# Kernel optimization log

Measured on AMD Instinct MI355X. Metric: run time of the kernel, lower is better.

Reference implementation:

```python
import jax, jax.numpy as jnp
import numpy as np

B, S, H, N_ITEMS = 1024, 200, 256, 50000


def setup_inputs() -> dict:
    key = jax.random.key(0)
    ks = jax.random.split(key, 10)
    s = 0.05
    x = jax.random.randint(ks[0], (B, S), 0, N_ITEMS)
    # timestamps: increasing along the sequence
    t = jnp.sort(jax.random.uniform(ks[1], (B, S), dtype=jnp.float32) * 10.0, axis=1)
    item_emb = (jax.random.normal(ks[2], (N_ITEMS, H), dtype=jnp.float32) * s).at[0].set(0.0)  # padding_idx=0
    W_ih = jax.random.normal(ks[3], (3 * H, H), dtype=jnp.float32) * s
    W_hh = jax.random.normal(ks[4], (3 * H, H), dtype=jnp.float32) * s
    b_ih = jnp.zeros((3 * H,), jnp.float32)
    b_hh = jnp.zeros((3 * H,), jnp.float32)
    W1 = jax.random.normal(ks[5], (H, H), dtype=jnp.float32) * s
    b1 = jnp.zeros((H,), jnp.float32)
    W2 = jax.random.normal(ks[6], (H, H), dtype=jnp.float32) * s
    b2 = jnp.zeros((H,), jnp.float32)
    W_head = jax.random.normal(ks[7], (N_ITEMS, H), dtype=jnp.float32) * s
    b_head = jnp.zeros((N_ITEMS,), jnp.float32)
    return dict(x=x, t=t, item_emb=item_emb, W_ih=W_ih, W_hh=W_hh, b_ih=b_ih,
                b_hh=b_hh, W1=W1, b1=b1, W2=W2, b2=b2, W_head=W_head, b_head=b_head)


def _gru_cell(xe, h, W_ih, W_hh, b_ih, b_hh):
    # PyTorch GRUCell: gates ordered (r, z, n)
    gi = xe @ W_ih.T + b_ih  # [B, 3H]
    gh = h @ W_hh.T + b_hh
    i_r, i_z, i_n = jnp.split(gi, 3, axis=-1)
    h_r, h_z, h_n = jnp.split(gh, 3, axis=-1)
    r = jax.nn.sigmoid(i_r + h_r)
    z = jax.nn.sigmoid(i_z + h_z)
    n = jnp.tanh(i_n + r * h_n)
    return (1.0 - z) * n + z * h


def _ode_f(h, W1, b1, W2, b2):
    # ODEFunc: MLP on hidden state (t-independent)
    return jnp.tanh(h @ W1.T + b1) @ W2.T + b2


def _rk4_step(h, dt, W1, b1, W2, b2):
    # dt: [B, 1]; dt == 0 on the last step => identity (matches i < seq_len-1 guard)
    f = lambda hh: _ode_f(hh, W1, b1, W2, b2)
    k1 = f(h)
    k2 = f(h + 0.5 * dt * k1)
    k3 = f(h + 0.5 * dt * k2)
    k4 = f(h + dt * k3)
    return h + (dt / 6.0) * (k1 + 2.0 * k2 + 2.0 * k3 + k4)


def reference(x, t, item_emb, W_ih, W_hh, b_ih, b_hh, W1, b1, W2, b2, W_head, b_head):
    x_emb = item_emb[x]  # [B, S, H]
    bsz = x.shape[0]
    # dt_i = max(t_{i+1}, t_i + 1e-5) - t_i for i < S-1, 0 for the final step
    t_next = jnp.maximum(t[:, 1:], t[:, :-1] + 1e-5)
    dt = jnp.concatenate([t_next - t[:, :-1], jnp.zeros((bsz, 1), t.dtype)], axis=1)  # [B, S]
    xs = (jnp.swapaxes(x_emb, 0, 1), jnp.swapaxes(dt, 0, 1)[..., None])  # [S,B,H], [S,B,1]
    h0 = jnp.zeros((bsz, x_emb.shape[-1]), x_emb.dtype)

    def step(h, inp):
        xe, dts = inp
        h = _gru_cell(xe, h, W_ih, W_hh, b_ih, b_hh)
        h = _rk4_step(h, dts, W1, b1, W2, b2)
        return h, None

    h, _ = jax.lax.scan(step, h0, xs)
    return h @ W_head.T + b_head  # [B, n_items]
```

## Files before the change

kernel.cpp:

```cpp
#include <hip/hip_runtime.h>


#define B_SZ   1024
#define S_LEN  200
#define HD     256
#define NITEMS 50000
#define NPAD   50048

#define OFF_WHH 0
#define OFF_WIH 196608
#define OFF_W1  393216
#define OFF_W2  458752
#define OFF_BHH 524288
#define OFF_BIH 525056
#define OFF_B1  525824
#define OFF_B2  526080
#define CANON_N 526336

typedef short short8 __attribute__((ext_vector_type(8)));
typedef float f32x4  __attribute__((ext_vector_type(4)));

__device__ __forceinline__ float bf2f(unsigned short u){
  unsigned v = ((unsigned)u) << 16; float f; __builtin_memcpy(&f, &v, 4); return f;
}
__device__ __forceinline__ unsigned short f2bf(float f){
  unsigned u; __builtin_memcpy(&u, &f, 4);
  u += 0x7FFFu + ((u >> 16) & 1u);
  return (unsigned short)(u >> 16);
}
__device__ __forceinline__ float fsig(float x){ return 1.0f / (1.0f + __expf(-x)); }
__device__ __forceinline__ float ftanh(float x){
  float e = __expf(-2.0f * fabsf(x));
  float r = (1.0f - e) / (1.0f + e);
  return copysignf(r, x);
}
__device__ __forceinline__ f32x4 MFMA(short8 a, short8 b, f32x4 c){
  return __builtin_amdgcn_mfma_f32_16x16x32_bf16(a, b, c, 0, 0, 0);
}
__device__ __forceinline__ int foff(int kc, int row){
  return (kc * 16 + ((row ^ kc) & 15)) * 8;
}

__global__ void sniff_kernel(const unsigned short* __restrict__ t, int* __restrict__ flag){
  int lane = threadIdx.x & 63;
  int bad = 0;
#pragma unroll
  for (int q = 0; q < 8; ++q)
    if (t[lane * 8 + q] > 0x4200u) bad = 1;
  unsigned long long m = __ballot(bad);
  if (lane == 0) flag[0] = (m != 0ull) ? 1 : 0;
}

__global__ void conv_kernel(const int* __restrict__ flag,
    const void* __restrict__ Whh, const void* __restrict__ Wih,
    const void* __restrict__ W1,  const void* __restrict__ W2,
    const void* __restrict__ bhh, const void* __restrict__ bih,
    const void* __restrict__ b1,  const void* __restrict__ b2,
    unsigned short* __restrict__ dst)
{
  int i = blockIdx.x * 256 + threadIdx.x;
  if (i >= CANON_N) return;
  int f32m = flag[0];
  const void* src; int off = i;
  if (i < OFF_WIH)      { src = Whh; off = i - OFF_WHH; }
  else if (i < OFF_W1)  { src = Wih; off = i - OFF_WIH; }
  else if (i < OFF_W2)  { src = W1;  off = i - OFF_W1; }
  else if (i < OFF_BHH) { src = W2;  off = i - OFF_W2; }
  else if (i < OFF_BIH) { src = bhh; off = i - OFF_BHH; }
  else if (i < OFF_B1)  { src = bih; off = i - OFF_BIH; }
  else if (i < OFF_B2)  { src = b1;  off = i - OFF_B1; }
  else                  { src = b2;  off = i - OFF_B2; }
  unsigned short v = f32m ? f2bf(((const float*)src)[off])
                          : ((const unsigned short*)src)[off];
  dst[i] = v;
}

__global__ void convw_kernel(const int* __restrict__ flag,
    const void* __restrict__ Wh, unsigned short* __restrict__ dst)
{
  int i4 = blockIdx.x * 256 + threadIdx.x;
  if (i4 * 4 >= NITEMS * HD) return;
  if (flag[0]){
    f32x4 v = ((const f32x4*)Wh)[i4];
#pragma unroll
    for (int q = 0; q < 4; ++q) dst[i4 * 4 + q] = f2bf(v[q]);
  } else {
    ((unsigned long long*)dst)[i4] = ((const unsigned long long*)Wh)[i4];
  }
}

__global__ void dt_kernel(const void* __restrict__ t, const int* __restrict__ flag,
                          float* __restrict__ dt){
  int i = blockIdx.x * 256 + threadIdx.x;
  if (i >= B_SZ * S_LEN) return;
  int f32m = flag[0];
  int s = i % S_LEN;
  float tc = f32m ? ((const float*)t)[i] : bf2f(((const unsigned short*)t)[i]);
  float d = 0.0f;
  if (s < S_LEN - 1){
    float tn = f32m ? ((const float*)t)[i + 1] : bf2f(((const unsigned short*)t)[i + 1]);
    d = fmaxf(tn, tc + 1e-5f) - tc;
  }
  dt[i] = d;
}

__global__ __launch_bounds__(256) void gitems_kernel(
    const void* __restrict__ emb, const unsigned short* __restrict__ canon,
    const int* __restrict__ flag, void* __restrict__ tbl, int tblf32)
{
  __shared__ __align__(16) short ap[4][4096];
  const int tid = threadIdx.x;
  const int i0 = blockIdx.x * 64;
  const int n0 = blockIdx.y * 256;
  const int f32m = flag[0];
  {
    int kc = tid & 31, r8 = tid >> 5;
#pragma unroll
    for (int p = 0; p < 8; ++p){
      int row = p * 8 + r8;
      int gr = i0 + row; if (gr > NITEMS - 1) gr = NITEMS - 1;
      short8 v;
      if (f32m){
        const f32x4* src = (const f32x4*)((const float*)emb + gr * HD + kc * 8);
        f32x4 v0 = src[0], v1 = src[1];
#pragma unroll
        for (int q = 0; q < 4; ++q){ v[q] = (short)f2bf(v0[q]); v[4+q] = (short)f2bf(v1[q]); }
      } else {
        v = *(const short8*)((const unsigned short*)emb + gr * HD + kc * 8);
      }
      *(short8*)&ap[row >> 4][foff(kc, row & 15)] = v;
    }
  }
  __syncthreads();
  const int wave = tid >> 6, lane = tid & 63, col = lane & 15, quad = lane >> 4;
  const unsigned short* Wih = canon + OFF_WIH;
  const unsigned short* bih = canon + OFF_BIH;
  f32x4 zz = {0.0f, 0.0f, 0.0f, 0.0f};
  f32x4 acc[4][4];
#pragma unroll
  for (int rt = 0; rt < 4; ++rt)
#pragma unroll
    for (int ct = 0; ct < 4; ++ct) acc[rt][ct] = zz;

#pragma unroll
  for (int ks = 0; ks < 8; ++ks){
    short8 bf[4];
#pragma unroll
    for (int ct = 0; ct < 4; ++ct){
      int n = n0 + wave * 64 + ct * 16 + col;
      bf[ct] = *(const short8*)(Wih + n * HD + ks * 32 + quad * 8);
    }
    int kc = ks * 4 + quad;
#pragma unroll
    for (int rt = 0; rt < 4; ++rt){
      short8 a = *(const short8*)&ap[rt][foff(kc, col)];
#pragma unroll
      for (int ct = 0; ct < 4; ++ct) acc[rt][ct] = MFMA(a, bf[ct], acc[rt][ct]);
    }
  }
  float bv[4];
#pragma unroll
  for (int ct = 0; ct < 4; ++ct) bv[ct] = bf2f(bih[n0 + wave * 64 + ct * 16 + col]);
  float* tfo = (float*)tbl; unsigned short* tbo = (unsigned short*)tbl;
#pragma unroll
  for (int rt = 0; rt < 4; ++rt)
#pragma unroll
    for (int ct = 0; ct < 4; ++ct)
#pragma unroll
      for (int r = 0; r < 4; ++r){
        int row = i0 + rt * 16 + quad * 4 + r;
        if (row < NITEMS){
          int n = n0 + wave * 64 + ct * 16 + col;
          float v = acc[rt][ct][r] + bv[ct];
          if (tblf32) tfo[row * 768 + n] = v;
          else        tbo[row * 768 + n] = (unsigned short)f2bf(v);
        }
      }
}

__global__ __launch_bounds__(512)
void scan_kernel(
    const int* __restrict__ x, const float* __restrict__ dtp,
    const unsigned short* __restrict__ canon,
    const void* __restrict__ tbl, int tblf32,
    float* __restrict__ hstate)
{
  __shared__ __align__(16) short bufhi[2][4096];
  __shared__ __align__(16) short buflo[2][4096];
  __shared__ __align__(16) int   xl[16 * S_LEN];
  __shared__ __align__(16) float dtall[16 * S_LEN];

  const int tid  = threadIdx.x;
  const int wave = tid >> 6;
  const int lane = tid & 63;
  const int col  = lane & 15;
  const int quad = lane >> 4;
  const int r0   = blockIdx.x * 16;
  const int wc0  = wave * 32;

  const unsigned short* Whh = canon + OFF_WHH;
  const unsigned short* W1w = canon + OFF_W1;
  const unsigned short* W2w = canon + OFF_W2;
  const unsigned short* bhh = canon + OFF_BHH;
  const unsigned short* b1v = canon + OFF_B1;
  const unsigned short* b2v = canon + OFF_B2;

  {
    short8 z = {0,0,0,0,0,0,0,0};
    *(short8*)&bufhi[0][tid * 8] = z;
    *(short8*)&buflo[0][tid * 8] = z;
  }
  for (int i = tid; i < 16 * S_LEN; i += 512){
    xl[i]    = x[r0 * S_LEN + i];
    dtall[i] = dtp[r0 * S_LEN + i];
  }

  float bR[2], bZ[2], bN[2], b1c[2], b2c[2];
#pragma unroll
  for (int ct = 0; ct < 2; ++ct){
    int c = wc0 + ct * 16 + col;
    bR[ct]  = bf2f(bhh[c]);          bZ[ct] = bf2f(bhh[HD + c]);
    bN[ct]  = bf2f(bhh[2 * HD + c]);
    b1c[ct] = bf2f(b1v[c]);          b2c[ct] = bf2f(b2v[c]);
  }

  float h[2][4];
#pragma unroll
  for (int ct = 0; ct < 2; ++ct)
#pragma unroll
    for (int r = 0; r < 4; ++r) h[ct][r] = 0.0f;

  const float* tf = (const float*)tbl;
  const unsigned short* tb = (const unsigned short*)tbl;

  __syncthreads();

  for (int s = 0; s < S_LEN; ++s){
    const int pb = s & 1;
    float dtr[4];
#pragma unroll
    for (int r = 0; r < 4; ++r) dtr[r] = dtall[(quad * 4 + r) * S_LEN + s];

    f32x4 aR[2], aZ[2], aN[2];
    float giN[2][4];
#pragma unroll
    for (int r = 0; r < 4; ++r){
      int row = quad * 4 + r;
      long base = (long)xl[row * S_LEN + s] * 768;
#pragma unroll
      for (int ct = 0; ct < 2; ++ct){
        int c = wc0 + ct * 16 + col;
        float gr, gz, gn;
        if (tblf32){
          gr = __builtin_nontemporal_load(tf + base + c);
          gz = __builtin_nontemporal_load(tf + base + 256 + c);
          gn = __builtin_nontemporal_load(tf + base + 512 + c);
        } else {
          gr = bf2f(__builtin_nontemporal_load(tb + base + c));
          gz = bf2f(__builtin_nontemporal_load(tb + base + 256 + c));
          gn = bf2f(__builtin_nontemporal_load(tb + base + 512 + c));
        }
        aR[ct][r] = gr; aZ[ct][r] = gz; aN[ct][r] = 0.0f; giN[ct][r] = gn;
      }
    }
#pragma unroll
    for (int ks = 0; ks < 8; ++ks){
      int kc = ks * 4 + quad;
      short8 ahi = *(const short8*)&bufhi[pb][foff(kc, col)];
      short8 alo = *(const short8*)&buflo[pb][foff(kc, col)];
#pragma unroll
      for (int ct = 0; ct < 2; ++ct){
        int nb = wc0 + ct * 16 + col;
        short8 b0 = *(const short8*)(Whh + (0 * HD + nb) * HD + ks * 32 + quad * 8);
        aR[ct] = MFMA(ahi, b0, aR[ct]); aR[ct] = MFMA(alo, b0, aR[ct]);
        short8 b1f = *(const short8*)(Whh + (1 * HD + nb) * HD + ks * 32 + quad * 8);
        aZ[ct] = MFMA(ahi, b1f, aZ[ct]); aZ[ct] = MFMA(alo, b1f, aZ[ct]);
        short8 b2f = *(const short8*)(Whh + (2 * HD + nb) * HD + ks * 32 + quad * 8);
        aN[ct] = MFMA(ahi, b2f, aN[ct]); aN[ct] = MFMA(alo, b2f, aN[ct]);
      }
    }
    float hg[2][4], ksum[2][4];
#pragma unroll
    for (int ct = 0; ct < 2; ++ct)
#pragma unroll
      for (int r = 0; r < 4; ++r){
        int row = quad * 4 + r;
        float rr = fsig(aR[ct][r] + bR[ct]);
        float z_ = fsig(aZ[ct][r] + bZ[ct]);
        float nn = ftanh(giN[ct][r] + rr * (aN[ct][r] + bN[ct]));
        float hgv = (1.0f - z_) * nn + z_ * h[ct][r];
        hg[ct][r] = hgv;
        int c = wc0 + ct * 16 + col;
        bufhi[1 - pb][foff(c >> 3, row) + (c & 7)] = (short)f2bf(hgv);
      }
    __syncthreads();

#pragma unroll
    for (int j = 0; j < 4; ++j){
      f32x4 ua[2];
      ua[0] = (f32x4){b1c[0], b1c[0], b1c[0], b1c[0]};
      ua[1] = (f32x4){b1c[1], b1c[1], b1c[1], b1c[1]};
#pragma unroll
      for (int ks = 0; ks < 8; ++ks){
        int kc = ks * 4 + quad;
        short8 a = *(const short8*)&bufhi[1 - pb][foff(kc, col)];
#pragma unroll
        for (int ct = 0; ct < 2; ++ct){
          short8 w = *(const short8*)(W1w + (wc0 + ct * 16 + col) * HD + ks * 32 + quad * 8);
          ua[ct] = MFMA(a, w, ua[ct]);
        }
      }
#pragma unroll
      for (int ct = 0; ct < 2; ++ct)
#pragma unroll
        for (int r = 0; r < 4; ++r){
          int row = quad * 4 + r, c = wc0 + ct * 16 + col;
          bufhi[pb][foff(c >> 3, row) + (c & 7)] = (short)f2bf(ftanh(ua[ct][r]));
        }
      __syncthreads();

      f32x4 ka[2];
      ka[0] = (f32x4){b2c[0], b2c[0], b2c[0], b2c[0]};
      ka[1] = (f32x4){b2c[1], b2c[1], b2c[1], b2c[1]};
#pragma unroll
      for (int ks = 0; ks < 8; ++ks){
        int kc = ks * 4 + quad;
        short8 a = *(const short8*)&bufhi[pb][foff(kc, col)];
#pragma unroll
        for (int ct = 0; ct < 2; ++ct){
          short8 w = *(const short8*)(W2w + (wc0 + ct * 16 + col) * HD + ks * 32 + quad * 8);
          ka[ct] = MFMA(a, w, ka[ct]);
        }
      }
#pragma unroll
      for (int ct = 0; ct < 2; ++ct)
#pragma unroll
        for (int r = 0; r < 4; ++r){
          int row = quad * 4 + r;
          float dtv = dtr[r];
          float kv = ka[ct][r];
          int c = wc0 + ct * 16 + col;
          if (j == 0){
            ksum[ct][r] = kv;
            float y = hg[ct][r] + 0.5f * dtv * kv;
            bufhi[1 - pb][foff(c >> 3, row) + (c & 7)] = (short)f2bf(y);
          } else if (j == 1){
            ksum[ct][r] += 2.0f * kv;
            float y = hg[ct][r] + 0.5f * dtv * kv;
            bufhi[1 - pb][foff(c >> 3, row) + (c & 7)] = (short)f2bf(y);
          } else if (j == 2){
            ksum[ct][r] += 2.0f * kv;
            float y = hg[ct][r] + dtv * kv;
            bufhi[1 - pb][foff(c >> 3, row) + (c & 7)] = (short)f2bf(y);
          } else {
            ksum[ct][r] += kv;
            float hn = hg[ct][r] + (dtv * (1.0f / 6.0f)) * ksum[ct][r];
            h[ct][r] = hn;
            unsigned short hh = f2bf(hn);
            float fh = bf2f(hh);
            unsigned short hl = f2bf(hn - fh);
            bufhi[1 - pb][foff(c >> 3, row) + (c & 7)] = (short)hh;
            buflo[1 - pb][foff(c >> 3, row) + (c & 7)] = (short)hl;
          }
        }
      __syncthreads();
    }
  }
#pragma unroll
  for (int ct = 0; ct < 2; ++ct)
#pragma unroll
    for (int r = 0; r < 4; ++r){
      int row = quad * 4 + r;
      hstate[(r0 + row) * HD + wc0 + ct * 16 + col] = h[ct][r];
    }
}

__global__ __launch_bounds__(256) void head_kernel(
    const float* __restrict__ hstate,
    const unsigned short* __restrict__ Whb,
    const void* __restrict__ Wh,
    const void* __restrict__ bh, const int* __restrict__ flag, int wbf,
    void* __restrict__ outv)
{
  __shared__ __align__(16) short ahi[4][4096];
  __shared__ __align__(16) short alo[4][4096];
  const int tid = threadIdx.x;
  const int i0 = blockIdx.x * 64;
  const int n0 = blockIdx.y * 256;
  const int f32m = flag[0];
  {
    int kc = tid & 31, r8 = tid >> 5;
#pragma unroll
    for (int p = 0; p < 8; ++p){
      int row = p * 8 + r8;
      const float* src = hstate + (i0 + row) * HD + kc * 8;
      short8 vh, vl;
#pragma unroll
      for (int q = 0; q < 8; ++q){
        float f = src[q];
        unsigned short hb = f2bf(f);
        float fh = bf2f(hb);
        vh[q] = (short)hb; vl[q] = (short)f2bf(f - fh);
      }
      int off = foff(kc, row & 15);
      *(short8*)&ahi[row >> 4][off] = vh;
      *(short8*)&alo[row >> 4][off] = vl;
    }
  }
  __syncthreads();
  const int wave = tid >> 6, lane = tid & 63, col = lane & 15, quad = lane >> 4;
  f32x4 zz = {0.0f, 0.0f, 0.0f, 0.0f};
  f32x4 acc[4][4];
#pragma unroll
  for (int rt = 0; rt < 4; ++rt)
#pragma unroll
    for (int ct = 0; ct < 4; ++ct) acc[rt][ct] = zz;

  int nidx[4];
#pragma unroll
  for (int ct = 0; ct < 4; ++ct){
    int n = n0 + wave * 64 + ct * 16 + col;
    nidx[ct] = (n < NITEMS) ? n : (NITEMS - 1);
  }
#pragma unroll
  for (int ks = 0; ks < 8; ++ks){
    short8 bf[4];
#pragma unroll
    for (int ct = 0; ct < 4; ++ct){
      if (wbf){
        bf[ct] = *(const short8*)(Whb + nidx[ct] * HD + ks * 32 + quad * 8);
      } else if (f32m){
        const f32x4* src = (const f32x4*)((const float*)Wh + nidx[ct] * HD + ks * 32 + quad * 8);
        f32x4 v0 = src[0], v1 = src[1];
        short8 v;
#pragma unroll
        for (int q = 0; q < 4; ++q){ v[q] = (short)f2bf(v0[q]); v[4+q] = (short)f2bf(v1[q]); }
        bf[ct] = v;
      } else {
        bf[ct] = *(const short8*)((const unsigned short*)Wh + nidx[ct] * HD + ks * 32 + quad * 8);
      }
    }
    int kc = ks * 4 + quad;
#pragma unroll
    for (int rt = 0; rt < 4; ++rt){
      short8 xh = *(const short8*)&ahi[rt][foff(kc, col)];
      short8 xl = *(const short8*)&alo[rt][foff(kc, col)];
#pragma unroll
      for (int ct = 0; ct < 4; ++ct){
        acc[rt][ct] = MFMA(xh, bf[ct], acc[rt][ct]);
        acc[rt][ct] = MFMA(xl, bf[ct], acc[rt][ct]);
      }
    }
  }
  float bhv[4];
#pragma unroll
  for (int ct = 0; ct < 4; ++ct)
    bhv[ct] = f32m ? ((const float*)bh)[nidx[ct]] : bf2f(((const unsigned short*)bh)[nidx[ct]]);
  float* outf = (float*)outv;
  unsigned short* outb = (unsigned short*)outv;
#pragma unroll
  for (int rt = 0; rt < 4; ++rt)
#pragma unroll
    for (int ct = 0; ct < 4; ++ct)
#pragma unroll
      for (int r = 0; r < 4; ++r){
        int row = i0 + rt * 16 + quad * 4 + r;
        int n = n0 + wave * 64 + ct * 16 + col;
        if (n < NITEMS){
          float v = acc[rt][ct][r] + bhv[ct];
          long o = (long)row * NITEMS + n;
          if (f32m) outf[o] = v;
          else      outb[o] = (unsigned short)f2bf(v);
        }
      }
}

extern "C" void kernel_launch(void* const* d_in, const int* in_sizes, int n_in,
                              void* d_out, int out_size, void* d_ws, size_t ws_size,
                              hipStream_t stream) {
  const int*  x     = (const int*)d_in[0];
  const void* t     = d_in[1];
  const void* emb   = d_in[2];
  const void* Wih   = d_in[3];
  const void* Whh   = d_in[4];
  const void* bih   = d_in[5];
  const void* bhh   = d_in[6];
  const void* W1    = d_in[7];
  const void* b1    = d_in[8];
  const void* W2    = d_in[9];
  const void* b2    = d_in[10];
  const void* Whead = d_in[11];
  const void* bhead = d_in[12];

  char* ws = (char*)d_ws;
  int*   flag   = (int*)(ws);
  float* dtbuf  = (float*)(ws + 4096);
  float* hstate = (float*)(ws + (1u << 20));
  unsigned short* canon = (unsigned short*)(ws + (2u << 20));
  unsigned short* wheadb = (unsigned short*)(ws + (4u << 20));
  const size_t tbase = 32u << 20;
  const size_t TBL_F32  = (size_t)NPAD * 768 * 4;
  const size_t TBL_BF16 = (size_t)NPAD * 768 * 2;

  int wbf = (ws_size >= (32u << 20)) ? 1 : 0;
  void* tbl; int tblf32;
  if (ws_size >= tbase + TBL_F32)       { tbl = (void*)(ws + tbase); tblf32 = 1; }
  else if (ws_size >= tbase + TBL_BF16) { tbl = (void*)(ws + tbase); tblf32 = 0; }
  else                                  { tbl = (void*)d_out;        tblf32 = 0; }

  sniff_kernel<<<dim3(1), dim3(64), 0, stream>>>((const unsigned short*)t, flag);
  conv_kernel<<<dim3((CANON_N + 255) / 256), dim3(256), 0, stream>>>(
      flag, Whh, Wih, W1, W2, bhh, bih, b1, b2, canon);
  if (wbf)
    convw_kernel<<<dim3((NITEMS * HD / 4 + 255) / 256), dim3(256), 0, stream>>>(
        flag, Whead, wheadb);
  dt_kernel<<<dim3((B_SZ * S_LEN + 255) / 256), dim3(256), 0, stream>>>(t, flag, dtbuf);
  gitems_kernel<<<dim3(NPAD / 64, 3), dim3(256), 0, stream>>>(emb, canon, flag, tbl, tblf32);
  scan_kernel<<<dim3(64), dim3(512), 0, stream>>>(x, dtbuf, canon, tbl, tblf32, hstate);
  head_kernel<<<dim3(B_SZ / 64, (NITEMS + 255) / 256), dim3(256), 0, stream>>>(
      hstate, wheadb, Whead, bhead, flag, wbf, d_out);
}
```

Before: 4.580 ms.

## Double the scan block to 1024 threads and prefetch weight fragments into registers

The scan kernel now runs 16 waves per block, and each wave owns a single 16-column tile instead of two, halving per-wave MFMA work along the serial recurrence. Weight fragments for the next matmul (Whh gates, W1, W2) are preloaded into two ping-pong register arrays, with sched_barriers placed so global weight loads overlap the current MFMAs instead of being issued inline. The time loop is unrolled by two to alternate the buffers. In exchange, register pressure per thread rises and barrier cost grows with more waves.

```diff
diff --git a/kernel.cpp b/kernel.cpp
--- a/kernel.cpp
+++ b/kernel.cpp
@@ -178,7 +178,105 @@
       }
 }
 
-__global__ __launch_bounds__(512)
+
+#define LDW(DST, PTR) \
+  _Pragma("unroll") for (int ks_ = 0; ks_ < 8; ++ks_) \
+    DST[ks_] = *(const short8*)((PTR) + ks_ * 32 + quad * 8);
+
+#define MM16(ACC, W, PB) \
+  _Pragma("unroll") for (int ks_ = 0; ks_ < 8; ++ks_){ \
+    int kc_ = ks_ * 4 + quad; \
+    short8 ahi_ = *(const short8*)&bufhi[PB][foff(kc_, col)]; \
+    short8 alo_ = *(const short8*)&buflo[PB][foff(kc_, col)]; \
+    ACC = MFMA(ahi_, W[ks_], ACC); \
+    ACC = MFMA(alo_, W[ks_], ACC); }
+
+#define RK4U(CUR, PRE, PPTR, PB) { \
+  LDW(PRE, PPTR); \
+  __builtin_amdgcn_sched_barrier(0); \
+  f32x4 ua_ = {b1c, b1c, b1c, b1c}; \
+  _Pragma("unroll") for (int ks_ = 0; ks_ < 8; ++ks_){ \
+    int kc_ = ks_ * 4 + quad; \
+    short8 a_ = *(const short8*)&bufhi[1-(PB)][foff(kc_, col)]; \
+    ua_ = MFMA(a_, CUR[ks_], ua_); } \
+  _Pragma("unroll") for (int r_ = 0; r_ < 4; ++r_){ \
+    int row_ = quad * 4 + r_; \
+    bufhi[PB][foff(cw >> 3, row_) + (cw & 7)] = (short)f2bf(ftanh(ua_[r_])); } }
+
+#define RK4K(CUR, PRE, PPTR, PB, J) { \
+  LDW(PRE, PPTR); \
+  __builtin_amdgcn_sched_barrier(0); \
+  f32x4 ka_ = {b2c, b2c, b2c, b2c}; \
+  _Pragma("unroll") for (int ks_ = 0; ks_ < 8; ++ks_){ \
+    int kc_ = ks_ * 4 + quad; \
+    short8 a_ = *(const short8*)&bufhi[PB][foff(kc_, col)]; \
+    ka_ = MFMA(a_, CUR[ks_], ka_); } \
+  _Pragma("unroll") for (int r_ = 0; r_ < 4; ++r_){ \
+    int row_ = quad * 4 + r_; \
+    float kv_ = ka_[r_]; \
+    if ((J) == 0) ksum[r_] = kv_; \
+    else if ((J) == 3) ksum[r_] += kv_; \
+    else ksum[r_] += 2.0f * kv_; \
+    if ((J) < 3){ \
+      float y_ = hg[r_] + (((J) == 2) ? dtr[r_] : 0.5f * dtr[r_]) * kv_; \
+      bufhi[1-(PB)][foff(cw >> 3, row_) + (cw & 7)] = (short)f2bf(y_); \
+    } else { \
+      float hn_ = hg[r_] + (dtr[r_] * (1.0f / 6.0f)) * ksum[r_]; \
+      h[r_] = hn_; \
+      unsigned short hh_ = f2bf(hn_); \
+      float fh_ = bf2f(hh_); \
+      bufhi[1-(PB)][foff(cw >> 3, row_) + (cw & 7)] = (short)hh_; \
+      buflo[1-(PB)][foff(cw >> 3, row_) + (cw & 7)] = (short)f2bf(hn_ - fh_); } } }
+
+#define STEP(WA, WB, PB, S) { \
+  float dtr[4]; \
+  _Pragma("unroll") for (int r_ = 0; r_ < 4; ++r_) \
+    dtr[r_] = dtall[(quad * 4 + r_) * S_LEN + (S)]; \
+  f32x4 aR = {0,0,0,0}, aZ = {0,0,0,0}, aN = {0,0,0,0}; \
+  float gRv[4], gZv[4], gNv[4]; \
+   \
+  LDW(WB, pZ); \
+  _Pragma("unroll") for (int r_ = 0; r_ < 4; ++r_){ \
+    long base_ = (long)xl[(quad * 4 + r_) * S_LEN + (S)] * 768; \
+    if (tblf32){ \
+      gRv[r_] = __builtin_nontemporal_load(tf + base_ + cw); \
+      gZv[r_] = __builtin_nontemporal_load(tf + base_ + 256 + cw); \
+      gNv[r_] = __builtin_nontemporal_load(tf + base_ + 512 + cw); \
+    } else { \
+      gRv[r_] = bf2f(__builtin_nontemporal_load(tb + base_ + cw)); \
+      gZv[r_] = bf2f(__builtin_nontemporal_load(tb + base_ + 256 + cw)); \
+      gNv[r_] = bf2f(__builtin_nontemporal_load(tb + base_ + 512 + cw)); } } \
+  __builtin_amdgcn_sched_barrier(0); \
+  MM16(aR, WA, PB); \
+   \
+  LDW(WA, pN); \
+  __builtin_amdgcn_sched_barrier(0); \
+  MM16(aZ, WB, PB); \
+   \
+  LDW(WB, p1); \
+  __builtin_amdgcn_sched_barrier(0); \
+  MM16(aN, WA, PB); \
+   \
+  float hg[4], ksum[4]; \
+  _Pragma("unroll") for (int r_ = 0; r_ < 4; ++r_){ \
+    int row_ = quad * 4 + r_; \
+    float rr_ = fsig(aR[r_] + gRv[r_] + bR); \
+    float z__ = fsig(aZ[r_] + gZv[r_] + bZ); \
+    float nn_ = ftanh(gNv[r_] + rr_ * (aN[r_] + bN)); \
+    float hgv_ = (1.0f - z__) * nn_ + z__ * h[r_]; \
+    hg[r_] = hgv_; \
+    bufhi[1-(PB)][foff(cw >> 3, row_) + (cw & 7)] = (short)f2bf(hgv_); } \
+  __syncthreads(); \
+  RK4U(WB, WA, p2, PB);      __syncthreads(); \
+  RK4K(WA, WB, p1, PB, 0);   __syncthreads(); \
+  RK4U(WB, WA, p2, PB);      __syncthreads(); \
+  RK4K(WA, WB, p1, PB, 1);   __syncthreads(); \
+  RK4U(WB, WA, p2, PB);      __syncthreads(); \
+  RK4K(WA, WB, p1, PB, 2);   __syncthreads(); \
+  RK4U(WB, WA, p2, PB);      __syncthreads(); \
+  RK4K(WA, WB, pR, PB, 3);   __syncthreads(); }
+
+__global__ __launch_bounds__(1024)
 void scan_kernel(
     const int* __restrict__ x, const float* __restrict__ dtp,
     const unsigned short* __restrict__ canon,
@@ -196,7 +294,7 @@
   const int col  = lane & 15;
   const int quad = lane >> 4;
   const int r0   = blockIdx.x * 16;
-  const int wc0  = wave * 32;
+  const int cw   = wave * 16 + col;
 
   const unsigned short* Whh = canon + OFF_WHH;
   const unsigned short* W1w = canon + OFF_W1;
@@ -205,174 +303,50 @@
   const unsigned short* b1v = canon + OFF_B1;
   const unsigned short* b2v = canon + OFF_B2;
 
-  {
+  const unsigned short* pR = Whh + (0 * HD + cw) * HD;
+  const unsigned short* pZ = Whh + (1 * HD + cw) * HD;
+  const unsigned short* pN = Whh + (2 * HD + cw) * HD;
+  const unsigned short* p1 = W1w + cw * HD;
+  const unsigned short* p2 = W2w + cw * HD;
+
+  if (tid < 512){
     short8 z = {0,0,0,0,0,0,0,0};
     *(short8*)&bufhi[0][tid * 8] = z;
     *(short8*)&buflo[0][tid * 8] = z;
   }
-  for (int i = tid; i < 16 * S_LEN; i += 512){
+  for (int i = tid; i < 16 * S_LEN; i += 1024){
     xl[i]    = x[r0 * S_LEN + i];
     dtall[i] = dtp[r0 * S_LEN + i];
   }
 
-  float bR[2], bZ[2], bN[2], b1c[2], b2c[2];
-#pragma unroll
-  for (int ct = 0; ct < 2; ++ct){
-    int c = wc0 + ct * 16 + col;
-    bR[ct]  = bf2f(bhh[c]);          bZ[ct] = bf2f(bhh[HD + c]);
-    bN[ct]  = bf2f(bhh[2 * HD + c]);
-    b1c[ct] = bf2f(b1v[c]);          b2c[ct] = bf2f(b2v[c]);
-  }
-
-  float h[2][4];
-#pragma unroll
-  for (int ct = 0; ct < 2; ++ct)
-#pragma unroll
-    for (int r = 0; r < 4; ++r) h[ct][r] = 0.0f;
+  const float bR  = bf2f(bhh[cw]);
+  const float bZ  = bf2f(bhh[HD + cw]);
+  const float bN  = bf2f(bhh[2 * HD + cw]);
+  const float b1c = bf2f(b1v[cw]);
+  const float b2c = bf2f(b2v[cw]);
+
+  float h[4];
+#pragma unroll
+  for (int r = 0; r < 4; ++r) h[r] = 0.0f;
 
   const float* tf = (const float*)tbl;
   const unsigned short* tb = (const unsigned short*)tbl;
 
+  short8 wA[8], wB[8];
+  LDW(wA, pR);
+
   __syncthreads();
 
-  for (int s = 0; s < S_LEN; ++s){
-    const int pb = s & 1;
-    float dtr[4];
-#pragma unroll
-    for (int r = 0; r < 4; ++r) dtr[r] = dtall[(quad * 4 + r) * S_LEN + s];
-
-    f32x4 aR[2], aZ[2], aN[2];
-    float giN[2][4];
-#pragma unroll
-    for (int r = 0; r < 4; ++r){
-      int row = quad * 4 + r;
-      long base = (long)xl[row * S_LEN + s] * 768;
-#pragma unroll
-      for (int ct = 0; ct < 2; ++ct){
-        int c = wc0 + ct * 16 + col;
-        float gr, gz, gn;
-        if (tblf32){
-          gr = __builtin_nontemporal_load(tf + base + c);
-          gz = __builtin_nontemporal_load(tf + base + 256 + c);
-          gn = __builtin_nontemporal_load(tf + base + 512 + c);
-        } else {
-          gr = bf2f(__builtin_nontemporal_load(tb + base + c));
-          gz = bf2f(__builtin_nontemporal_load(tb + base + 256 + c));
-          gn = bf2f(__builtin_nontemporal_load(tb + base + 512 + c));
-        }
-        aR[ct][r] = gr; aZ[ct][r] = gz; aN[ct][r] = 0.0f; giN[ct][r] = gn;
-      }
-    }
-#pragma unroll
-    for (int ks = 0; ks < 8; ++ks){
-      int kc = ks * 4 + quad;
-      short8 ahi = *(const short8*)&bufhi[pb][foff(kc, col)];
-      short8 alo = *(const short8*)&buflo[pb][foff(kc, col)];
-#pragma unroll
-      for (int ct = 0; ct < 2; ++ct){
-        int nb = wc0 + ct * 16 + col;
-        short8 b0 = *(const short8*)(Whh + (0 * HD + nb) * HD + ks * 32 + quad * 8);
-        aR[ct] = MFMA(ahi, b0, aR[ct]); aR[ct] = MFMA(alo, b0, aR[ct]);
-        short8 b1f = *(const short8*)(Whh + (1 * HD + nb) * HD + ks * 32 + quad * 8);
-        aZ[ct] = MFMA(ahi, b1f, aZ[ct]); aZ[ct] = MFMA(alo, b1f, aZ[ct]);
-        short8 b2f = *(const short8*)(Whh + (2 * HD + nb) * HD + ks * 32 + quad * 8);
-        aN[ct] = MFMA(ahi, b2f, aN[ct]); aN[ct] = MFMA(alo, b2f, aN[ct]);
-      }
-    }
-    float hg[2][4], ksum[2][4];
-#pragma unroll
-    for (int ct = 0; ct < 2; ++ct)
-#pragma unroll
-      for (int r = 0; r < 4; ++r){
-        int row = quad * 4 + r;
-        float rr = fsig(aR[ct][r] + bR[ct]);
-        float z_ = fsig(aZ[ct][r] + bZ[ct]);
-        float nn = ftanh(giN[ct][r] + rr * (aN[ct][r] + bN[ct]));
-        float hgv = (1.0f - z_) * nn + z_ * h[ct][r];
-        hg[ct][r] = hgv;
-        int c = wc0 + ct * 16 + col;
-        bufhi[1 - pb][foff(c >> 3, row) + (c & 7)] = (short)f2bf(hgv);
-      }
-    __syncthreads();
-
-#pragma unroll
-    for (int j = 0; j < 4; ++j){
-      f32x4 ua[2];
-      ua[0] = (f32x4){b1c[0], b1c[0], b1c[0], b1c[0]};
-      ua[1] = (f32x4){b1c[1], b1c[1], b1c[1], b1c[1]};
-#pragma unroll
-      for (int ks = 0; ks < 8; ++ks){
-        int kc = ks * 4 + quad;
-        short8 a = *(const short8*)&bufhi[1 - pb][foff(kc, col)];
-#pragma unroll
-        for (int ct = 0; ct < 2; ++ct){
-          short8 w = *(const short8*)(W1w + (wc0 + ct * 16 + col) * HD + ks * 32 + quad * 8);
-          ua[ct] = MFMA(a, w, ua[ct]);
-        }
-      }
-#pragma unroll
-      for (int ct = 0; ct < 2; ++ct)
-#pragma unroll
-        for (int r = 0; r < 4; ++r){
-          int row = quad * 4 + r, c = wc0 + ct * 16 + col;
-          bufhi[pb][foff(c >> 3, row) + (c & 7)] = (short)f2bf(ftanh(ua[ct][r]));
-        }
-      __syncthreads();
-
-      f32x4 ka[2];
-      ka[0] = (f32x4){b2c[0], b2c[0], b2c[0], b2c[0]};
-      ka[1] = (f32x4){b2c[1], b2c[1], b2c[1], b2c[1]};
-#pragma unroll
-      for (int ks = 0; ks < 8; ++ks){
-        int kc = ks * 4 + quad;
-        short8 a = *(const short8*)&bufhi[pb][foff(kc, col)];
-#pragma unroll
-        for (int ct = 0; ct < 2; ++ct){
-          short8 w = *(const short8*)(W2w + (wc0 + ct * 16 + col) * HD + ks * 32 + quad * 8);
-          ka[ct] = MFMA(a, w, ka[ct]);
-        }
-      }
-#pragma unroll
-      for (int ct = 0; ct < 2; ++ct)
-#pragma unroll
-        for (int r = 0; r < 4; ++r){
-          int row = quad * 4 + r;
-          float dtv = dtr[r];
-          float kv = ka[ct][r];
-          int c = wc0 + ct * 16 + col;
-          if (j == 0){
-            ksum[ct][r] = kv;
-            float y = hg[ct][r] + 0.5f * dtv * kv;
-            bufhi[1 - pb][foff(c >> 3, row) + (c & 7)] = (short)f2bf(y);
-          } else if (j == 1){
-            ksum[ct][r] += 2.0f * kv;
-            float y = hg[ct][r] + 0.5f * dtv * kv;
-            bufhi[1 - pb][foff(c >> 3, row) + (c & 7)] = (short)f2bf(y);
-          } else if (j == 2){
-            ksum[ct][r] += 2.0f * kv;
-            float y = hg[ct][r] + dtv * kv;
-            bufhi[1 - pb][foff(c >> 3, row) + (c & 7)] = (short)f2bf(y);
-          } else {
-            ksum[ct][r] += kv;
-            float hn = hg[ct][r] + (dtv * (1.0f / 6.0f)) * ksum[ct][r];
-            h[ct][r] = hn;
-            unsigned short hh = f2bf(hn);
-            float fh = bf2f(hh);
-            unsigned short hl = f2bf(hn - fh);
-            bufhi[1 - pb][foff(c >> 3, row) + (c & 7)] = (short)hh;
-            buflo[1 - pb][foff(c >> 3, row) + (c & 7)] = (short)hl;
-          }
-        }
-      __syncthreads();
-    }
-  }
-#pragma unroll
-  for (int ct = 0; ct < 2; ++ct)
-#pragma unroll
-    for (int r = 0; r < 4; ++r){
-      int row = quad * 4 + r;
-      hstate[(r0 + row) * HD + wc0 + ct * 16 + col] = h[ct][r];
-    }
+  for (int s = 0; s < S_LEN; s += 2){
+    STEP(wA, wB, 0, s);
+    STEP(wB, wA, 1, s + 1);
+  }
+
+#pragma unroll
+  for (int r = 0; r < 4; ++r){
+    int row = quad * 4 + r;
+    hstate[(r0 + row) * HD + cw] = h[r];
+  }
 }
 
 __global__ __launch_bounds__(256) void head_kernel(
@@ -444,11 +418,11 @@
 #pragma unroll
     for (int rt = 0; rt < 4; ++rt){
       short8 xh = *(const short8*)&ahi[rt][foff(kc, col)];
-      short8 xl = *(const short8*)&alo[rt][foff(kc, col)];
+      short8 xl2 = *(const short8*)&alo[rt][foff(kc, col)];
 #pragma unroll
       for (int ct = 0; ct < 4; ++ct){
         acc[rt][ct] = MFMA(xh, bf[ct], acc[rt][ct]);
-        acc[rt][ct] = MFMA(xl, bf[ct], acc[rt][ct]);
+        acc[rt][ct] = MFMA(xl2, bf[ct], acc[rt][ct]);
       }
     }
   }
@@ -516,7 +490,7 @@
         flag, Whead, wheadb);
   dt_kernel<<<dim3((B_SZ * S_LEN + 255) / 256), dim3(256), 0, stream>>>(t, flag, dtbuf);
   gitems_kernel<<<dim3(NPAD / 64, 3), dim3(256), 0, stream>>>(emb, canon, flag, tbl, tblf32);
-  scan_kernel<<<dim3(64), dim3(512), 0, stream>>>(x, dtbuf, canon, tbl, tblf32, hstate);
+  scan_kernel<<<dim3(64), dim3(1024), 0, stream>>>(x, dtbuf, canon, tbl, tblf32, hstate);
   head_kernel<<<dim3(B_SZ / 64, (NITEMS + 255) / 256), dim3(256), 0, stream>>>(
       hstate, wheadb, Whead, bhead, flag, wbf, d_out);
 }
```

Result: slower. 6.101 ms (+33.2%).
